# Kernel tuning notes

Hardware: AMD Instinct MI355X
Metric: run time of the kernel (lower is better)

The kernel has to match this reference:

```python
import jax, jax.numpy as jnp
import numpy as np

B, C, H, W = 8, 64, 128, 128
CH = 3 * C      # MS_CAM channels = channels*3 = 192
IC = CH // 2    # inter_channels with r=2 = 96
EPS = 1e-5


def _conv1x1(x, w, b):
    # x: [B, Cin, H, W], w: [Cout, Cin], b: [Cout]
    return jnp.einsum('bchw,oc->bohw', x, w) + b[:, None, None]


def _bn(x, g, beta, mean, var):
    # eval-mode BatchNorm2d over channel axis 1
    scale = g / jnp.sqrt(var + EPS)
    return (x - mean[:, None, None]) * scale[:, None, None] + beta[:, None, None]


def setup_inputs() -> dict:
    key = jax.random.key(0)
    ks = jax.random.split(key, 24)
    f = lambda i, s, sc=1.0: jax.random.normal(ks[i], s, jnp.float32) * sc
    d = {
        'x1': f(0, (B, C, H, W)),
        'x2': f(1, (B, C, H, W)),
        'x3': f(2, (B, C, H, W)),
    }
    def make_path(prefix, off):
        d[prefix + 'w1'] = f(off + 0, (IC, CH), 0.05)
        d[prefix + 'b1'] = f(off + 1, (IC,), 0.05)
        d[prefix + 'g1'] = jnp.ones((IC,), jnp.float32)
        d[prefix + 'be1'] = jnp.zeros((IC,), jnp.float32)
        d[prefix + 'm1'] = f(off + 2, (IC,), 0.05)
        d[prefix + 'v1'] = jax.random.uniform(ks[off + 3], (IC,), jnp.float32) + 0.5
        d[prefix + 'w2'] = f(off + 4, (CH, IC), 0.05)
        d[prefix + 'b2'] = f(off + 5, (CH,), 0.05)
        d[prefix + 'g2'] = jnp.ones((CH,), jnp.float32)
        d[prefix + 'be2'] = jnp.zeros((CH,), jnp.float32)
        d[prefix + 'm2'] = f(off + 6, (CH,), 0.05)
        d[prefix + 'v2'] = jax.random.uniform(ks[off + 7], (CH,), jnp.float32) + 0.5
    make_path('l', 3)   # local_att params
    make_path('g', 12)  # global_att params
    return d


def _att_branch(x, w1, b1, g1, be1, m1, v1, w2, b2, g2, be2, m2, v2):
    h = jax.nn.relu(_bn(_conv1x1(x, w1, b1), g1, be1, m1, v1))
    return _bn(_conv1x1(h, w2, b2), g2, be2, m2, v2)


def reference(x1, x2, x3,
              lw1, lb1, lg1, lbe1, lm1, lv1, lw2, lb2, lg2, lbe2, lm2, lv2,
              gw1, gb1, gg1, gbe1, gm1, gv1, gw2, gb2, gg2, gbe2, gm2, gv2):
    # MS_CAM: concat, local (per-pixel) + global (GAP) channel attention
    x = jnp.concatenate([x1, x2, x3], axis=1)                      # [B, 3C, H, W]
    xl = _att_branch(x, lw1, lb1, lg1, lbe1, lm1, lv1, lw2, lb2, lg2, lbe2, lm2, lv2)
    xg = _att_branch(jnp.mean(x, axis=(2, 3), keepdims=True),      # [B, 3C, 1, 1]
                     gw1, gb1, gg1, gbe1, gm1, gv1, gw2, gb2, gg2, gbe2, gm2, gv2)
    wei = jax.nn.sigmoid(xl + xg)                                  # [B, 3C, H, W]

    # FUB edge/node matrices + per-pixel 1x3 @ 3x1 bmm collapse to a fused
    # softmax-over-3 weighted sum (identical flatten order on both sides).
    w = jnp.stack([wei[:, 0:C], wei[:, C:2 * C], wei[:, 2 * C:]], axis=0)  # [3,B,C,H,W]
    w = jax.nn.softmax(w, axis=0)
    xs = jnp.stack([x1, x2, x3], axis=0)                           # [3,B,C,H,W]
    return jnp.sum(w * xs, axis=0)                                 # [B,C,H,W]
```

## Files before the change

kernel.cpp:

```cpp
#include <hip/hip_runtime.h>

#define HWPIX 16384
#define XSTR 200
#define HSTR 104
#define L2E 1.4426950408889634f

typedef float f32x4 __attribute__((ext_vector_type(4)));
typedef short s16x8 __attribute__((ext_vector_type(8)));

static __device__ __forceinline__ unsigned short f2bf(float f) {
    unsigned int u = __builtin_bit_cast(unsigned int, f);
    u += 0x7fffu + ((u >> 16) & 1u);
    return (unsigned short)(u >> 16);
}
static __device__ __forceinline__ unsigned int pack2(float lo, float hi) {
    return (unsigned int)f2bf(lo) | ((unsigned int)f2bf(hi) << 16);
}
static __device__ __forceinline__ unsigned int cvtpk(float lo, float hi) {
    unsigned int r;
    asm("v_cvt_pk_bf16_f32 %0, %1, %2" : "=v"(r) : "v"(lo), "v"(hi));
    return r;
}


__global__ __launch_bounds__(256) void prep_kernel(
    const float* __restrict__ x1, const float* __restrict__ x2, const float* __restrict__ x3,
    const float* __restrict__ lw1, const float* __restrict__ lb1,
    const float* __restrict__ lg1, const float* __restrict__ lbe1,
    const float* __restrict__ lm1, const float* __restrict__ lv1,
    const float* __restrict__ lw2, const float* __restrict__ lb2,
    const float* __restrict__ lg2, const float* __restrict__ lbe2,
    const float* __restrict__ lm2, const float* __restrict__ lv2,
    float* __restrict__ wsf, unsigned short* __restrict__ w1f, unsigned short* __restrict__ w2f)
{
    const int bid = blockIdx.x, t = threadIdx.x;
    if (bid < 1536) {
        int b = bid / 192, c = bid % 192;
        int g = c >> 6, cc = c & 63;
        const float* base = (g == 0 ? x1 : (g == 1 ? x2 : x3)) + ((size_t)(b * 64 + cc)) * HWPIX;
        float s = 0.f;
        #pragma unroll
        for (int it = 0; it < 16; ++it) {
            f32x4 v = *(const f32x4*)(base + it * 1024 + t * 4);
            s += v[0] + v[1] + v[2] + v[3];
        }
        for (int off = 32; off > 0; off >>= 1) s += __shfl_down(s, off, 64);
        __shared__ float part[4];
        if ((t & 63) == 0) part[t >> 6] = s;
        __syncthreads();
        if (t == 0) wsf[bid] = (part[0] + part[1] + part[2] + part[3]) * (1.f / (float)HWPIX);
    } else if (bid == 1536) {
        if (t < 96) {
            float s = lg1[t] * __frsqrt_rn(lv1[t] + 1e-5f);
            wsf[3072 + t] = s;
            wsf[3168 + t] = (lb1[t] - lm1[t]) * s + lbe1[t];
        }
    } else if (bid == 1537) {
        if (t < 192) {
            float s = lg2[t] * __frsqrt_rn(lv2[t] + 1e-5f);
            wsf[3264 + t] = s;
            wsf[3456 + t] = (lb2[t] - lm2[t]) * s + lbe2[t];
        }
    } else if (bid < 1547) {
        int slot = (bid - 1538) * 256 + t;
        int f = slot >> 6, l = slot & 63;
        int kb = f / 6, nb = f % 6;
        int row = nb * 16 + (l & 15), col0 = kb * 32 + ((l >> 4) << 3);
        const float* src = lw1 + row * 192 + col0;
        f32x4 a = *(const f32x4*)src, b4 = *(const f32x4*)(src + 4);
        unsigned int* dst = (unsigned int*)(w1f + f * 512 + l * 8);
        dst[0] = pack2(a[0], a[1]); dst[1] = pack2(a[2], a[3]);
        dst[2] = pack2(b4[0], b4[1]); dst[3] = pack2(b4[2], b4[3]);
    } else {
        int slot = (bid - 1547) * 256 + t;
        int f = slot >> 6, l = slot & 63;
        int kb = f / 12, nb = f % 12;
        int row = nb * 16 + (l & 15), col0 = kb * 32 + ((l >> 4) << 3);
        const float* src = lw2 + row * 96 + col0;
        f32x4 a = *(const f32x4*)src, b4 = *(const f32x4*)(src + 4);
        unsigned int* dst = (unsigned int*)(w2f + f * 512 + l * 8);
        dst[0] = pack2(a[0], a[1]); dst[1] = pack2(a[2], a[3]);
        dst[2] = pack2(b4[0], b4[1]); dst[3] = pack2(b4[2], b4[3]);
    }
}

__global__ __launch_bounds__(256) void gpath_kernel(
    const float* __restrict__ gw1, const float* __restrict__ gb1,
    const float* __restrict__ gg1, const float* __restrict__ gbe1,
    const float* __restrict__ gm1, const float* __restrict__ gv1,
    const float* __restrict__ gw2, const float* __restrict__ gb2,
    const float* __restrict__ gg2, const float* __restrict__ gbe2,
    const float* __restrict__ gm2, const float* __restrict__ gv2,
    float* __restrict__ wsf)
{
    __shared__ float xbar[192], hbuf[96];
    const int b = blockIdx.x, t = threadIdx.x;
    if (t < 192) xbar[t] = wsf[b * 192 + t];
    __syncthreads();
    if (t < 96) {
        float acc = 0.f;
        #pragma unroll 8
        for (int c = 0; c < 192; ++c) acc += gw1[t * 192 + c] * xbar[c];
        float s = gg1[t] * __frsqrt_rn(gv1[t] + 1e-5f);
        float tt = (gb1[t] - gm1[t]) * s + gbe1[t];
        hbuf[t] = fmaxf(acc * s + tt, 0.f);
    }
    __syncthreads();
    if (t < 192) {
        float acc = 0.f;
        #pragma unroll 8
        for (int j = 0; j < 96; ++j) acc += gw2[t * 96 + j] * hbuf[j];
        float s = gg2[t] * __frsqrt_rn(gv2[t] + 1e-5f);
        float tt = (gb2[t] - gm2[t]) * s + gbe2[t];
        wsf[1536 + b * 192 + t] = acc * s + tt;
    }
}

__global__ __launch_bounds__(256, 4) void main_kernel(
    const float* __restrict__ x1, const float* __restrict__ x2, const float* __restrict__ x3,
    const float* __restrict__ wsf,
    const unsigned short* __restrict__ w1f, const unsigned short* __restrict__ w2f,
    float* __restrict__ out)
{
    __shared__ __align__(16) unsigned short lx[64 * XSTR];
    __shared__ float lpar[576];

    const int t = threadIdx.x;
    const int b = blockIdx.x >> 8;
    const int pix0 = (blockIdx.x & 255) << 6;
    const int lane = t & 63;
    const int wv = t >> 6;
    const int col = lane & 15;
    const int q = lane >> 4;
    const int pixw = wv * 16;

    const unsigned short* wb1 = w1f + lane * 8;
    const unsigned short* wb2 = w2f + lane * 8;

    f32x4 va[6], vb[6];
    {
        const int pq = t >> 4;
        const int cb = t & 15;
        #pragma unroll
        for (int i = 0; i < 6; ++i) {
            int cp = i * 16 + cb;
            int c0 = cp * 2;
            int g = c0 >> 6, cc0 = c0 & 63;
            const float* pl = (g == 0 ? x1 : (g == 1 ? x2 : x3))
                + ((size_t)(b * 64 + cc0)) * HWPIX + pix0 + pq * 4;
            va[i] = *(const f32x4*)pl;
            vb[i] = *(const f32x4*)(pl + HWPIX);
        }
    }

    s16x8 wcur[6];
    #pragma unroll
    for (int nb = 0; nb < 6; ++nb) wcur[nb] = *(const s16x8*)(wb1 + nb * 512);

    if (t < 96)  { lpar[t] = wsf[3072 + t]; lpar[96 + t] = wsf[3168 + t]; }
    if (t < 192) {
        float s2 = wsf[3264 + t], t2 = wsf[3456 + t], xg = wsf[1536 + b * 192 + t];
        lpar[192 + t] = -L2E * s2;
        lpar[384 + t] = -L2E * (t2 + xg);
    }
    {
        const int pq = t >> 4;
        const int cb = t & 15;
        unsigned int* lx32 = (unsigned int*)lx;
        #pragma unroll
        for (int i = 0; i < 6; ++i) {
            int cp = i * 16 + cb;
            #pragma unroll
            for (int j = 0; j < 4; ++j)
                lx32[(pq * 4 + j) * 100 + cp] = cvtpk(va[i][j], vb[i][j]);
        }
    }
    __syncthreads();

    unsigned short* lhp = &lx[pixw * XSTR];

    s16x8 a1[6];
    #pragma unroll
    for (int kb = 0; kb < 6; ++kb)
        a1[kb] = *(const s16x8*)&lx[(pixw + col) * XSTR + kb * 32 + q * 8];

    f32x4 acc1[6];
    #pragma unroll
    for (int nb = 0; nb < 6; ++nb) acc1[nb] = (f32x4){0.f, 0.f, 0.f, 0.f};

    s16x8 wnxt[6];
    #pragma unroll
    for (int kb = 0; kb < 6; ++kb) {
        if (kb < 5) {
            #pragma unroll
            for (int nb = 0; nb < 6; ++nb)
                wnxt[nb] = *(const s16x8*)(wb1 + ((kb + 1) * 6 + nb) * 512);
        }
        #pragma unroll
        for (int nb = 0; nb < 6; ++nb)
            acc1[nb] = __builtin_amdgcn_mfma_f32_16x16x32_bf16(a1[kb], wcur[nb], acc1[nb], 0, 0, 0);
        if (kb < 5) {
            #pragma unroll
            for (int nb = 0; nb < 6; ++nb) wcur[nb] = wnxt[nb];
        }
    }

    s16x8 v2cur[6];
    #pragma unroll
    for (int i = 0; i < 6; ++i) v2cur[i] = *(const s16x8*)(wb2 + i * 512);

    #pragma unroll
    for (int nbp = 0; nbp < 3; ++nbp) {
        int j0 = (2 * nbp) * 16 + col, j1 = (2 * nbp + 1) * 16 + col;
        float s0 = lpar[j0], t0 = lpar[96 + j0];
        float s1v = lpar[j1], t1v = lpar[96 + j1];
        #pragma unroll
        for (int r = 0; r < 4; ++r) {
            float h0 = fmaxf(acc1[2 * nbp][r] * s0 + t0, 0.f);
            float h1 = fmaxf(acc1[2 * nbp + 1][r] * s1v + t1v, 0.f);
            unsigned int w = cvtpk(h0, h1);
            int rowo = (q * 4 + r) * HSTR;
            lhp[rowo + j0] = (unsigned short)w;
            lhp[rowo + j1] = (unsigned short)(w >> 16);
        }
    }

    s16x8 a2[3];
    #pragma unroll
    for (int kb = 0; kb < 3; ++kb)
        a2[kb] = *(const s16x8*)&lhp[col * HSTR + kb * 32 + q * 8];

    f32x4 acc2[12];
    #pragma unroll
    for (int nb = 0; nb < 12; ++nb) acc2[nb] = (f32x4){0.f, 0.f, 0.f, 0.f};

    s16x8 v2nxt[6];
    #pragma unroll
    for (int h = 0; h < 6; ++h) {
        int kb = h >> 1, nbo = (h & 1) * 6;
        if (h < 5) {
            #pragma unroll
            for (int i = 0; i < 6; ++i)
                v2nxt[i] = *(const s16x8*)(wb2 + ((h + 1) * 6 + i) * 512);
        }
        #pragma unroll
        for (int i = 0; i < 6; ++i)
            acc2[nbo + i] = __builtin_amdgcn_mfma_f32_16x16x32_bf16(a2[kb], v2cur[i], acc2[nbo + i], 0, 0, 0);
        if (h < 5) {
            #pragma unroll
            for (int i = 0; i < 6; ++i) v2cur[i] = v2nxt[i];
        }
    }

    f32x4 xa[4], xb4[4], xc4[4];
    size_t po[4];
    #pragma unroll
    for (int nb = 0; nb < 4; ++nb) {
        int cc = nb * 16 + col;
        po[nb] = ((size_t)(b * 64 + cc)) * HWPIX + pix0 + pixw + q * 4;
        xa[nb]  = *(const f32x4*)(x1 + po[nb]);
        xb4[nb] = *(const f32x4*)(x2 + po[nb]);
        xc4[nb] = *(const f32x4*)(x3 + po[nb]);
    }
    #pragma unroll
    for (int nb = 0; nb < 4; ++nb) {
        int cc = nb * 16 + col;
        float A0 = lpar[192 + cc],       B0 = lpar[384 + cc];
        float A1 = lpar[192 + 64 + cc],  B1 = lpar[384 + 64 + cc];
        float A2 = lpar[192 + 128 + cc], B2 = lpar[384 + 128 + cc];
        f32x4 res;
        #pragma unroll
        for (int r = 0; r < 4; ++r) {
            float w0 = __builtin_amdgcn_rcpf(1.f + __builtin_amdgcn_exp2f(acc2[nb][r]     * A0 + B0));
            float w1 = __builtin_amdgcn_rcpf(1.f + __builtin_amdgcn_exp2f(acc2[nb + 4][r] * A1 + B1));
            float w2 = __builtin_amdgcn_rcpf(1.f + __builtin_amdgcn_exp2f(acc2[nb + 8][r] * A2 + B2));
            float e0 = __builtin_amdgcn_exp2f(w0 * L2E);
            float e1 = __builtin_amdgcn_exp2f(w1 * L2E);
            float e2 = __builtin_amdgcn_exp2f(w2 * L2E);
            float inv = __builtin_amdgcn_rcpf(e0 + e1 + e2);
            res[r] = (e0 * xa[nb][r] + e1 * xb4[nb][r] + e2 * xc4[nb][r]) * inv;
        }
        *(f32x4*)(out + po[nb]) = res;
    }
}

extern "C" void kernel_launch(void* const* d_in, const int* in_sizes, int n_in,
                              void* d_out, int out_size, void* d_ws, size_t ws_size,
                              hipStream_t stream) {
    (void)in_sizes; (void)n_in; (void)out_size; (void)ws_size;
    const float* x1  = (const float*)d_in[0];
    const float* x2  = (const float*)d_in[1];
    const float* x3  = (const float*)d_in[2];
    const float* lw1 = (const float*)d_in[3];
    const float* lb1 = (const float*)d_in[4];
    const float* lg1 = (const float*)d_in[5];
    const float* lbe1= (const float*)d_in[6];
    const float* lm1 = (const float*)d_in[7];
    const float* lv1 = (const float*)d_in[8];
    const float* lw2 = (const float*)d_in[9];
    const float* lb2 = (const float*)d_in[10];
    const float* lg2 = (const float*)d_in[11];
    const float* lbe2= (const float*)d_in[12];
    const float* lm2 = (const float*)d_in[13];
    const float* lv2 = (const float*)d_in[14];
    const float* gw1 = (const float*)d_in[15];
    const float* gb1 = (const float*)d_in[16];
    const float* gg1 = (const float*)d_in[17];
    const float* gbe1= (const float*)d_in[18];
    const float* gm1 = (const float*)d_in[19];
    const float* gv1 = (const float*)d_in[20];
    const float* gw2 = (const float*)d_in[21];
    const float* gb2 = (const float*)d_in[22];
    const float* gg2 = (const float*)d_in[23];
    const float* gbe2= (const float*)d_in[24];
    const float* gm2 = (const float*)d_in[25];
    const float* gv2 = (const float*)d_in[26];

    float* wsf = (float*)d_ws;
    unsigned short* w1f = (unsigned short*)((char*)d_ws + 16384);
    unsigned short* w2f = w1f + 18432;

    prep_kernel<<<1556, 256, 0, stream>>>(x1, x2, x3,
        lw1, lb1, lg1, lbe1, lm1, lv1, lw2, lb2, lg2, lbe2, lm2, lv2,
        wsf, w1f, w2f);
    gpath_kernel<<<8, 256, 0, stream>>>(
        gw1, gb1, gg1, gbe1, gm1, gv1, gw2, gb2, gg2, gbe2, gm2, gv2, wsf);
    main_kernel<<<2048, 256, 0, stream>>>(x1, x2, x3, wsf, w1f, w2f, (float*)d_out);
}
```

Before: 230.0 us.

## Double-buffer MFMA weight loads with sched barriers and drop block barrier

```diff
diff --git a/kernel.cpp b/kernel.cpp
--- a/kernel.cpp
+++ b/kernel.cpp
@@ -21,6 +21,8 @@
     asm("v_cvt_pk_bf16_f32 %0, %1, %2" : "=v"(r) : "v"(lo), "v"(hi));
     return r;
 }
+
+#define SBAR() __builtin_amdgcn_sched_barrier(0)
 
 
 __global__ __launch_bounds__(256) void prep_kernel(
@@ -116,14 +118,13 @@
     }
 }
 
-__global__ __launch_bounds__(256, 4) void main_kernel(
+__global__ __launch_bounds__(256, 6) void main_kernel(
     const float* __restrict__ x1, const float* __restrict__ x2, const float* __restrict__ x3,
     const float* __restrict__ wsf,
     const unsigned short* __restrict__ w1f, const unsigned short* __restrict__ w2f,
     float* __restrict__ out)
 {
     __shared__ __align__(16) unsigned short lx[64 * XSTR];
-    __shared__ float lpar[576];
 
     const int t = threadIdx.x;
     const int b = blockIdx.x >> 8;
@@ -133,39 +134,40 @@
     const int col = lane & 15;
     const int q = lane >> 4;
     const int pixw = wv * 16;
+    const int pq = t >> 4;
+    const int cb = t & 15;
 
     const unsigned short* wb1 = w1f + lane * 8;
     const unsigned short* wb2 = w2f + lane * 8;
 
+#define LD6(W, BASE, SET)                                                   \
+    _Pragma("unroll")                                                       \
+    for (int i_ = 0; i_ < 6; ++i_)                                          \
+        W[i_] = *(const s16x8*)((BASE) + ((SET) * 6 + i_) * 512);
+#define MF6_1(AK, W)                                                        \
+    _Pragma("unroll")                                                       \
+    for (int n_ = 0; n_ < 6; ++n_)                                          \
+        acc1[n_] = __builtin_amdgcn_mfma_f32_16x16x32_bf16(AK, W[n_], acc1[n_], 0, 0, 0);
+#define MF6_2(AK, W, NBO)                                                   \
+    _Pragma("unroll")                                                       \
+    for (int n_ = 0; n_ < 6; ++n_)                                          \
+        acc2[(NBO) + n_] = __builtin_amdgcn_mfma_f32_16x16x32_bf16(AK, W[n_], acc2[(NBO) + n_], 0, 0, 0);
+
     f32x4 va[6], vb[6];
+    #pragma unroll
+    for (int i = 0; i < 6; ++i) {
+        int cp = i * 16 + cb, c0 = cp * 2;
+        int g = c0 >> 6, cc0 = c0 & 63;
+        const float* pl = (g == 0 ? x1 : (g == 1 ? x2 : x3))
+            + ((size_t)(b * 64 + cc0)) * HWPIX + pix0 + pq * 4;
+        va[i] = *(const f32x4*)pl;
+        vb[i] = *(const f32x4*)(pl + HWPIX);
+    }
+    s16x8 wA[6], wB[6];
+    LD6(wA, wb1, 0);
+    SBAR();
+
     {
-        const int pq = t >> 4;
-        const int cb = t & 15;
-        #pragma unroll
-        for (int i = 0; i < 6; ++i) {
-            int cp = i * 16 + cb;
-            int c0 = cp * 2;
-            int g = c0 >> 6, cc0 = c0 & 63;
-            const float* pl = (g == 0 ? x1 : (g == 1 ? x2 : x3))
-                + ((size_t)(b * 64 + cc0)) * HWPIX + pix0 + pq * 4;
-            va[i] = *(const f32x4*)pl;
-            vb[i] = *(const f32x4*)(pl + HWPIX);
-        }
-    }
-
-    s16x8 wcur[6];
-    #pragma unroll
-    for (int nb = 0; nb < 6; ++nb) wcur[nb] = *(const s16x8*)(wb1 + nb * 512);
-
-    if (t < 96)  { lpar[t] = wsf[3072 + t]; lpar[96 + t] = wsf[3168 + t]; }
-    if (t < 192) {
-        float s2 = wsf[3264 + t], t2 = wsf[3456 + t], xg = wsf[1536 + b * 192 + t];
-        lpar[192 + t] = -L2E * s2;
-        lpar[384 + t] = -L2E * (t2 + xg);
-    }
-    {
-        const int pq = t >> 4;
-        const int cb = t & 15;
         unsigned int* lx32 = (unsigned int*)lx;
         #pragma unroll
         for (int i = 0; i < 6; ++i) {
@@ -175,49 +177,46 @@
                 lx32[(pq * 4 + j) * 100 + cp] = cvtpk(va[i][j], vb[i][j]);
         }
     }
-    __syncthreads();
-
-    unsigned short* lhp = &lx[pixw * XSTR];
 
     s16x8 a1[6];
     #pragma unroll
     for (int kb = 0; kb < 6; ++kb)
         a1[kb] = *(const s16x8*)&lx[(pixw + col) * XSTR + kb * 32 + q * 8];
 
+    LD6(wB, wb1, 1);
+    float s1v[6], t1v[6];
+    #pragma unroll
+    for (int nb = 0; nb < 6; ++nb) {
+        int j = nb * 16 + col;
+        s1v[nb] = wsf[3072 + j]; t1v[nb] = wsf[3168 + j];
+    }
+    float s2v[12], t2v[12], xgv[12];
+    #pragma unroll
+    for (int i = 0; i < 12; ++i) {
+        int c = i * 16 + col;
+        s2v[i] = wsf[3264 + c]; t2v[i] = wsf[3456 + c]; xgv[i] = wsf[1536 + b * 192 + c];
+    }
+    SBAR();
+
     f32x4 acc1[6];
     #pragma unroll
     for (int nb = 0; nb < 6; ++nb) acc1[nb] = (f32x4){0.f, 0.f, 0.f, 0.f};
 
-    s16x8 wnxt[6];
-    #pragma unroll
-    for (int kb = 0; kb < 6; ++kb) {
-        if (kb < 5) {
-            #pragma unroll
-            for (int nb = 0; nb < 6; ++nb)
-                wnxt[nb] = *(const s16x8*)(wb1 + ((kb + 1) * 6 + nb) * 512);
-        }
-        #pragma unroll
-        for (int nb = 0; nb < 6; ++nb)
-            acc1[nb] = __builtin_amdgcn_mfma_f32_16x16x32_bf16(a1[kb], wcur[nb], acc1[nb], 0, 0, 0);
-        if (kb < 5) {
-            #pragma unroll
-            for (int nb = 0; nb < 6; ++nb) wcur[nb] = wnxt[nb];
-        }
-    }
-
-    s16x8 v2cur[6];
-    #pragma unroll
-    for (int i = 0; i < 6; ++i) v2cur[i] = *(const s16x8*)(wb2 + i * 512);
-
+    MF6_1(a1[0], wA);
+    LD6(wA, wb1, 2); SBAR(); MF6_1(a1[1], wB);
+    LD6(wB, wb1, 3); SBAR(); MF6_1(a1[2], wA);
+    LD6(wA, wb1, 4); SBAR(); MF6_1(a1[3], wB);
+    LD6(wB, wb1, 5); SBAR(); MF6_1(a1[4], wA);
+    LD6(wA, wb2, 0); SBAR(); MF6_1(a1[5], wB);
+
+    unsigned short* lhp = &lx[pixw * XSTR];
     #pragma unroll
     for (int nbp = 0; nbp < 3; ++nbp) {
         int j0 = (2 * nbp) * 16 + col, j1 = (2 * nbp + 1) * 16 + col;
-        float s0 = lpar[j0], t0 = lpar[96 + j0];
-        float s1v = lpar[j1], t1v = lpar[96 + j1];
         #pragma unroll
         for (int r = 0; r < 4; ++r) {
-            float h0 = fmaxf(acc1[2 * nbp][r] * s0 + t0, 0.f);
-            float h1 = fmaxf(acc1[2 * nbp + 1][r] * s1v + t1v, 0.f);
+            float h0 = fmaxf(acc1[2 * nbp][r]     * s1v[2 * nbp]     + t1v[2 * nbp], 0.f);
+            float h1 = fmaxf(acc1[2 * nbp + 1][r] * s1v[2 * nbp + 1] + t1v[2 * nbp + 1], 0.f);
             unsigned int w = cvtpk(h0, h1);
             int rowo = (q * 4 + r) * HSTR;
             lhp[rowo + j0] = (unsigned short)w;
@@ -229,29 +228,7 @@
     #pragma unroll
     for (int kb = 0; kb < 3; ++kb)
         a2[kb] = *(const s16x8*)&lhp[col * HSTR + kb * 32 + q * 8];
-
-    f32x4 acc2[12];
-    #pragma unroll
-    for (int nb = 0; nb < 12; ++nb) acc2[nb] = (f32x4){0.f, 0.f, 0.f, 0.f};
-
-    s16x8 v2nxt[6];
-    #pragma unroll
-    for (int h = 0; h < 6; ++h) {
-        int kb = h >> 1, nbo = (h & 1) * 6;
-        if (h < 5) {
-            #pragma unroll
-            for (int i = 0; i < 6; ++i)
-                v2nxt[i] = *(const s16x8*)(wb2 + ((h + 1) * 6 + i) * 512);
-        }
-        #pragma unroll
-        for (int i = 0; i < 6; ++i)
-            acc2[nbo + i] = __builtin_amdgcn_mfma_f32_16x16x32_bf16(a2[kb], v2cur[i], acc2[nbo + i], 0, 0, 0);
-        if (h < 5) {
-            #pragma unroll
-            for (int i = 0; i < 6; ++i) v2cur[i] = v2nxt[i];
-        }
-    }
-
+    LD6(wB, wb2, 1);
     f32x4 xa[4], xb4[4], xc4[4];
     size_t po[4];
     #pragma unroll
@@ -262,18 +239,33 @@
         xb4[nb] = *(const f32x4*)(x2 + po[nb]);
         xc4[nb] = *(const f32x4*)(x3 + po[nb]);
     }
+    SBAR();
+
+    f32x4 acc2[12];
+    #pragma unroll
+    for (int nb = 0; nb < 12; ++nb) acc2[nb] = (f32x4){0.f, 0.f, 0.f, 0.f};
+
+    MF6_2(a2[0], wA, 0);
+    LD6(wA, wb2, 2); SBAR(); MF6_2(a2[0], wB, 6);
+    LD6(wB, wb2, 3); SBAR(); MF6_2(a2[1], wA, 0);
+    LD6(wA, wb2, 4); SBAR(); MF6_2(a2[1], wB, 6);
+    LD6(wB, wb2, 5); SBAR(); MF6_2(a2[2], wA, 0);
+    SBAR();          MF6_2(a2[2], wB, 6);
+
+    float Ap[12], Bp[12];
+    #pragma unroll
+    for (int i = 0; i < 12; ++i) {
+        Ap[i] = -L2E * s2v[i];
+        Bp[i] = -L2E * (t2v[i] + xgv[i]);
+    }
     #pragma unroll
     for (int nb = 0; nb < 4; ++nb) {
-        int cc = nb * 16 + col;
-        float A0 = lpar[192 + cc],       B0 = lpar[384 + cc];
-        float A1 = lpar[192 + 64 + cc],  B1 = lpar[384 + 64 + cc];
-        float A2 = lpar[192 + 128 + cc], B2 = lpar[384 + 128 + cc];
         f32x4 res;
         #pragma unroll
         for (int r = 0; r < 4; ++r) {
-            float w0 = __builtin_amdgcn_rcpf(1.f + __builtin_amdgcn_exp2f(acc2[nb][r]     * A0 + B0));
-            float w1 = __builtin_amdgcn_rcpf(1.f + __builtin_amdgcn_exp2f(acc2[nb + 4][r] * A1 + B1));
-            float w2 = __builtin_amdgcn_rcpf(1.f + __builtin_amdgcn_exp2f(acc2[nb + 8][r] * A2 + B2));
+            float w0 = __builtin_amdgcn_rcpf(1.f + __builtin_amdgcn_exp2f(acc2[nb][r]     * Ap[nb]     + Bp[nb]));
+            float w1 = __builtin_amdgcn_rcpf(1.f + __builtin_amdgcn_exp2f(acc2[nb + 4][r] * Ap[nb + 4] + Bp[nb + 4]));
+            float w2 = __builtin_amdgcn_rcpf(1.f + __builtin_amdgcn_exp2f(acc2[nb + 8][r] * Ap[nb + 8] + Bp[nb + 8]));
             float e0 = __builtin_amdgcn_exp2f(w0 * L2E);
             float e1 = __builtin_amdgcn_exp2f(w1 * L2E);
             float e2 = __builtin_amdgcn_exp2f(w2 * L2E);
@@ -282,6 +274,9 @@
         }
         *(f32x4*)(out + po[nb]) = res;
     }
+#undef LD6
+#undef MF6_1
+#undef MF6_2
 }
 
 extern "C" void kernel_launch(void* const* d_in, const int* in_sizes, int n_in,
```

After: 472.4 us. 105% more time.

## Shrink main kernel blocks to two waves and drop the block barrier

Applied to the files above, without the earlier changes.

```diff
diff --git a/kernel.cpp b/kernel.cpp
--- a/kernel.cpp
+++ b/kernel.cpp
@@ -116,18 +116,17 @@
     }
 }
 
-__global__ __launch_bounds__(256, 4) void main_kernel(
+__global__ __launch_bounds__(128) void main_kernel(
     const float* __restrict__ x1, const float* __restrict__ x2, const float* __restrict__ x3,
     const float* __restrict__ wsf,
     const unsigned short* __restrict__ w1f, const unsigned short* __restrict__ w2f,
     float* __restrict__ out)
 {
-    __shared__ __align__(16) unsigned short lx[64 * XSTR];
-    __shared__ float lpar[576];
+    __shared__ __align__(16) unsigned short lx[32 * XSTR];
 
     const int t = threadIdx.x;
-    const int b = blockIdx.x >> 8;
-    const int pix0 = (blockIdx.x & 255) << 6;
+    const int b = blockIdx.x >> 9;
+    const int pix0 = (blockIdx.x & 511) << 5;
     const int lane = t & 63;
     const int wv = t >> 6;
     const int col = lane & 15;
@@ -138,44 +137,39 @@
     const unsigned short* wb2 = w2f + lane * 8;
 
     f32x4 va[6], vb[6];
+    const int pq = t >> 4;
+    const int cb = t & 15;
+    #pragma unroll
+    for (int i = 0; i < 6; ++i) {
+        int cp = i * 16 + cb;
+        int c0 = cp * 2;
+        int g = c0 >> 6, cc0 = c0 & 63;
+        const float* pl = (g == 0 ? x1 : (g == 1 ? x2 : x3))
+            + ((size_t)(b * 64 + cc0)) * HWPIX + pix0 + pq * 4;
+        va[i] = *(const f32x4*)pl;
+        vb[i] = *(const f32x4*)(pl + HWPIX);
+    }
+
+    s16x8 wcur[6];
+    #pragma unroll
+    for (int nb = 0; nb < 6; ++nb) wcur[nb] = *(const s16x8*)(wb1 + nb * 512);
+    float s1v[6], t1v[6];
+    #pragma unroll
+    for (int nb = 0; nb < 6; ++nb) {
+        int j = nb * 16 + col;
+        s1v[nb] = wsf[3072 + j]; t1v[nb] = wsf[3168 + j];
+    }
+
     {
-        const int pq = t >> 4;
-        const int cb = t & 15;
+        unsigned int* lx32 = (unsigned int*)lx;
         #pragma unroll
         for (int i = 0; i < 6; ++i) {
             int cp = i * 16 + cb;
-            int c0 = cp * 2;
-            int g = c0 >> 6, cc0 = c0 & 63;
-            const float* pl = (g == 0 ? x1 : (g == 1 ? x2 : x3))
-                + ((size_t)(b * 64 + cc0)) * HWPIX + pix0 + pq * 4;
-            va[i] = *(const f32x4*)pl;
-            vb[i] = *(const f32x4*)(pl + HWPIX);
-        }
-    }
-
-    s16x8 wcur[6];
-    #pragma unroll
-    for (int nb = 0; nb < 6; ++nb) wcur[nb] = *(const s16x8*)(wb1 + nb * 512);
-
-    if (t < 96)  { lpar[t] = wsf[3072 + t]; lpar[96 + t] = wsf[3168 + t]; }
-    if (t < 192) {
-        float s2 = wsf[3264 + t], t2 = wsf[3456 + t], xg = wsf[1536 + b * 192 + t];
-        lpar[192 + t] = -L2E * s2;
-        lpar[384 + t] = -L2E * (t2 + xg);
-    }
-    {
-        const int pq = t >> 4;
-        const int cb = t & 15;
-        unsigned int* lx32 = (unsigned int*)lx;
-        #pragma unroll
-        for (int i = 0; i < 6; ++i) {
-            int cp = i * 16 + cb;
             #pragma unroll
             for (int j = 0; j < 4; ++j)
                 lx32[(pq * 4 + j) * 100 + cp] = cvtpk(va[i][j], vb[i][j]);
         }
     }
-    __syncthreads();
 
     unsigned short* lhp = &lx[pixw * XSTR];
 
@@ -212,12 +206,10 @@
     #pragma unroll
     for (int nbp = 0; nbp < 3; ++nbp) {
         int j0 = (2 * nbp) * 16 + col, j1 = (2 * nbp + 1) * 16 + col;
-        float s0 = lpar[j0], t0 = lpar[96 + j0];
-        float s1v = lpar[j1], t1v = lpar[96 + j1];
         #pragma unroll
         for (int r = 0; r < 4; ++r) {
-            float h0 = fmaxf(acc1[2 * nbp][r] * s0 + t0, 0.f);
-            float h1 = fmaxf(acc1[2 * nbp + 1][r] * s1v + t1v, 0.f);
+            float h0 = fmaxf(acc1[2 * nbp][r]     * s1v[2 * nbp]     + t1v[2 * nbp], 0.f);
+            float h1 = fmaxf(acc1[2 * nbp + 1][r] * s1v[2 * nbp + 1] + t1v[2 * nbp + 1], 0.f);
             unsigned int w = cvtpk(h0, h1);
             int rowo = (q * 4 + r) * HSTR;
             lhp[rowo + j0] = (unsigned short)w;
@@ -252,6 +244,14 @@
         }
     }
 
+    float Ap[12], Bp[12];
+    #pragma unroll
+    for (int i = 0; i < 12; ++i) {
+        int c = i * 16 + col;
+        float s2 = wsf[3264 + c], t2 = wsf[3456 + c], xg = wsf[1536 + b * 192 + c];
+        Ap[i] = -L2E * s2;
+        Bp[i] = -L2E * (t2 + xg);
+    }
     f32x4 xa[4], xb4[4], xc4[4];
     size_t po[4];
     #pragma unroll
@@ -264,16 +264,12 @@
     }
     #pragma unroll
     for (int nb = 0; nb < 4; ++nb) {
-        int cc = nb * 16 + col;
-        float A0 = lpar[192 + cc],       B0 = lpar[384 + cc];
-        float A1 = lpar[192 + 64 + cc],  B1 = lpar[384 + 64 + cc];
-        float A2 = lpar[192 + 128 + cc], B2 = lpar[384 + 128 + cc];
         f32x4 res;
         #pragma unroll
         for (int r = 0; r < 4; ++r) {
-            float w0 = __builtin_amdgcn_rcpf(1.f + __builtin_amdgcn_exp2f(acc2[nb][r]     * A0 + B0));
-            float w1 = __builtin_amdgcn_rcpf(1.f + __builtin_amdgcn_exp2f(acc2[nb + 4][r] * A1 + B1));
-            float w2 = __builtin_amdgcn_rcpf(1.f + __builtin_amdgcn_exp2f(acc2[nb + 8][r] * A2 + B2));
+            float w0 = __builtin_amdgcn_rcpf(1.f + __builtin_amdgcn_exp2f(acc2[nb][r]     * Ap[nb]     + Bp[nb]));
+            float w1 = __builtin_amdgcn_rcpf(1.f + __builtin_amdgcn_exp2f(acc2[nb + 4][r] * Ap[nb + 4] + Bp[nb + 4]));
+            float w2 = __builtin_amdgcn_rcpf(1.f + __builtin_amdgcn_exp2f(acc2[nb + 8][r] * Ap[nb + 8] + Bp[nb + 8]));
             float e0 = __builtin_amdgcn_exp2f(w0 * L2E);
             float e1 = __builtin_amdgcn_exp2f(w1 * L2E);
             float e2 = __builtin_amdgcn_exp2f(w2 * L2E);
@@ -325,5 +321,5 @@
         wsf, w1f, w2f);
     gpath_kernel<<<8, 256, 0, stream>>>(
         gw1, gb1, gg1, gbe1, gm1, gv1, gw2, gb2, gg2, gbe2, gm2, gv2, wsf);
-    main_kernel<<<2048, 256, 0, stream>>>(x1, x2, x3, wsf, w1f, w2f, (float*)d_out);
-}
+    main_kernel<<<4096, 128, 0, stream>>>(x1, x2, x3, wsf, w1f, w2f, (float*)d_out);
+}
```

Result: slower. 235.7 us (+2.5%).
